# Optimization experiments

Hardware: AMD Instinct MI355X
Metric: run time of the kernel (lower is better)

The kernel has to match this reference:

```python
import jax, jax.numpy as jnp
import numpy as np

N, E, F_IN, H, L = 100000, 1600000, 256, 128, 4
ALPHA, THETA, EPS = 0.1, 0.5, 1e-5


def setup_inputs() -> dict:
    key = jax.random.key(0)
    ks = jax.random.split(key, 6)
    x = jax.random.normal(ks[0], (N, F_IN), dtype=jnp.float32)
    edge_index = jax.random.randint(ks[1], (2, E), 0, N, dtype=jnp.int32)
    lin0_w = jax.random.normal(ks[2], (F_IN, H), dtype=jnp.float32) / np.sqrt(F_IN)
    lin0_b = jnp.zeros((H,), dtype=jnp.float32)
    conv_w = jax.random.normal(ks[3], (L, H, H), dtype=jnp.float32) / np.sqrt(H)
    bn_gamma = jnp.ones((L - 1, H), dtype=jnp.float32)
    bn_beta = jnp.zeros((L - 1, H), dtype=jnp.float32)
    return {"x": x, "edge_index": edge_index, "lin0_w": lin0_w, "lin0_b": lin0_b,
            "conv_w": conv_w, "bn_gamma": bn_gamma, "bn_beta": bn_beta}


def reference(x, edge_index, lin0_w, lin0_b, conv_w, bn_gamma, bn_beta):
    n = x.shape[0]
    loops = jnp.arange(n, dtype=edge_index.dtype)
    row = jnp.concatenate([edge_index[0], loops])  # source
    col = jnp.concatenate([edge_index[1], loops])  # target
    # GCN symmetric normalization with self-loops: D^{-1/2}(A+I)D^{-1/2}
    deg = jax.ops.segment_sum(jnp.ones_like(col, dtype=x.dtype), col, num_segments=n)
    dinv = jnp.where(deg > 0, jax.lax.rsqrt(deg), 0.0)
    norm = (dinv[row] * dinv[col])[:, None]  # [E+N, 1]

    def prop(h):  # sparse aggregation: out[c] += norm * h[r]
        return jax.ops.segment_sum(h[row] * norm, col, num_segments=n)

    # GCNConv input layer
    z = prop(x @ lin0_w) + lin0_b
    x0 = z
    for i in range(L):
        h = prop(z)
        beta = float(np.log(THETA / (i + 1) + 1.0))
        s = (1.0 - ALPHA) * h + ALPHA * x0          # identity mapping to initial features
        z = (1.0 - beta) * s + beta * (s @ conv_w[i])  # shared_weights GCN2Conv
        if i < L - 1:
            mu = jnp.mean(z, axis=0)
            var = jnp.mean((z - mu) ** 2, axis=0)
            z = (z - mu) * jax.lax.rsqrt(var + EPS) * bn_gamma[i] + bn_beta[i]
            z = jax.nn.relu(z)
    return z
```

## Files before the change

kernel.cpp:

```cpp
#include <hip/hip_runtime.h>
#include <hip/hip_bf16.h>
#include <math.h>

#define H 128
#define EPS_BN 1e-5f
#define RSTATS 16

typedef __attribute__((ext_vector_type(8))) short short8;
typedef __attribute__((ext_vector_type(4))) float f32x4;

__device__ __forceinline__ float bf2f(ushort u){
  union { float f; uint v; } x; x.v = ((uint)u) << 16; return x.f;
}
__device__ __forceinline__ ushort f2bf(float f){
  union { float f; uint v; } x; x.f = f;
  uint v = x.v;
  uint r = v + 0x7fff + ((v >> 16) & 1);
  return (ushort)(r >> 16);
}

__device__ __forceinline__ void acc8(float* a, uint4 v, float wt){
  a[0] += wt*bf2f((ushort)(v.x & 0xffff)); a[1] += wt*bf2f((ushort)(v.x >> 16));
  a[2] += wt*bf2f((ushort)(v.y & 0xffff)); a[3] += wt*bf2f((ushort)(v.y >> 16));
  a[4] += wt*bf2f((ushort)(v.z & 0xffff)); a[5] += wt*bf2f((ushort)(v.z >> 16));
  a[6] += wt*bf2f((ushort)(v.w & 0xffff)); a[7] += wt*bf2f((ushort)(v.w >> 16));
}


__global__ void k_count(const int* __restrict__ col, int E, int* __restrict__ cnt){
  int i = blockIdx.x*blockDim.x + threadIdx.x;
  if (i < E) atomicAdd(&cnt[col[i]], 1);
}

__global__ void k_scan1(const int* __restrict__ cnt, int* __restrict__ off,
                        int* __restrict__ bsum, float* __restrict__ dinv, int n){
  __shared__ int s[1024];
  int t = threadIdx.x;
  int i = blockIdx.x*1024 + t;
  int v = (i < n) ? cnt[i] : 0;
  if (i < n) dinv[i] = rsqrtf((float)v + 1.0f);
  s[t] = v; __syncthreads();
  for (int d = 1; d < 1024; d <<= 1){
    int x = (t >= d) ? s[t-d] : 0;
    __syncthreads();
    s[t] += x;
    __syncthreads();
  }
  if (i < n) off[i] = s[t] - v;
  if (t == 1023) bsum[blockIdx.x] = s[1023];
}

__global__ void k_scan2(int* bsum, int nb){
  int l = threadIdx.x;
  int carry = 0;
  for (int b0 = 0; b0 < nb; b0 += 64){
    int i = b0 + l;
    int orig = (i < nb) ? bsum[i] : 0;
    int v = orig;
    #pragma unroll
    for (int d = 1; d < 64; d <<= 1){
      int x = __shfl_up(v, d);
      if (l >= d) v += x;
    }
    if (i < nb) bsum[i] = carry + v - orig;
    carry += __shfl(v, 63);
  }
}

__global__ void k_scan3(int* __restrict__ off, int* __restrict__ cursor,
                        const int* __restrict__ bsum, int n, int Etot){
  int i = blockIdx.x*blockDim.x + threadIdx.x;
  if (i < n){ int o = off[i] + bsum[i >> 10]; off[i] = o; cursor[i] = o; }
  if (i == 0) off[n] = Etot;
}

__global__ void k_fill(const int* __restrict__ row, const int* __restrict__ col, int E,
                       const float* __restrict__ dinv, int* __restrict__ cursor,
                       uint2* __restrict__ edge){
  int i = blockIdx.x*blockDim.x + threadIdx.x;
  if (i < E){
    int c = col[i], r = row[i];
    int p = atomicAdd(&cursor[c], 1);
    edge[p] = make_uint2((uint)r, __float_as_uint(dinv[r]*dinv[c]));
  }
}


__global__ __launch_bounds__(1024) void k_dhist(
    const int* __restrict__ cnt, int* __restrict__ dh, int n){
  __shared__ int lh[256];
  int t = threadIdx.x;
  if (t < 256) lh[t] = 0;
  __syncthreads();
  int i = blockIdx.x*1024 + t;
  if (i < n){
    int d = cnt[i]; if (d > 255) d = 255;
    atomicAdd(&lh[d], 1);
  }
  __syncthreads();
  if (t < 256 && lh[t]) atomicAdd(&dh[t], lh[t]);
}

__global__ void k_dscan(int* __restrict__ dh){
  __shared__ int s[256];
  int t = threadIdx.x;
  int v = dh[t];
  s[t] = v; __syncthreads();
  for (int d = 1; d < 256; d <<= 1){
    int x = (t >= d) ? s[t-d] : 0;
    __syncthreads();
    s[t] += x;
    __syncthreads();
  }
  dh[t] = s[t] - v;
}

__global__ __launch_bounds__(1024) void k_dperm(
    const int* __restrict__ cnt, int* __restrict__ dh,
    int* __restrict__ perm, int n){
  __shared__ int lh[256];
  __shared__ int lbase[256];
  int t = threadIdx.x;
  if (t < 256) lh[t] = 0;
  __syncthreads();
  int i = blockIdx.x*1024 + t;
  int d = 0, li = 0;
  if (i < n){
    d = cnt[i]; if (d > 255) d = 255;
    li = atomicAdd(&lh[d], 1);
  }
  __syncthreads();
  if (t < 256){
    int c = lh[t];
    lbase[t] = c ? atomicAdd(&dh[t], c) : 0;
  }
  __syncthreads();
  if (i < n) perm[lbase[d] + li] = i;
}


__global__ void k_prepw(const float* __restrict__ lin0_w, const float* __restrict__ conv_w,
                        ushort* __restrict__ lin0T, ushort* __restrict__ WpT,
                        float b0, float b1, float b2, float b3){
  int i = blockIdx.x*blockDim.x + threadIdx.x;
  if (i < 128*256){
    int nn = i >> 8, k = i & 255;
    lin0T[i] = f2bf(lin0_w[k*128 + nn]);
  } else if (i < 128*256 + 4*128*128){
    int j = i - 128*256;
    int ll = j >> 14, rc = j & 16383;
    int nn = rc >> 7, k = rc & 127;
    float beta = (ll==0)?b0:(ll==1)?b1:(ll==2)?b2:b3;
    float v = beta * conv_w[ll*16384 + k*128 + nn];
    if (k == nn) v += 1.0f - beta;
    WpT[j] = f2bf(v);
  }
}


__device__ __forceinline__ void gather_edges(
    float* a, const ushort* __restrict__ zin, const uint2* __restrict__ edge,
    int e0, int e1, int lr){
  int e = e0;
  for (; e + 3 < e1; e += 4){
    uint2 er0 = edge[e],   er1 = edge[e+1];
    uint2 er2 = edge[e+2], er3 = edge[e+3];
    uint4 v0 = *(const uint4*)(zin + (size_t)er0.x*H + lr*8);
    uint4 v1 = *(const uint4*)(zin + (size_t)er1.x*H + lr*8);
    uint4 v2 = *(const uint4*)(zin + (size_t)er2.x*H + lr*8);
    uint4 v3 = *(const uint4*)(zin + (size_t)er3.x*H + lr*8);
    acc8(a, v0, __uint_as_float(er0.y));
    acc8(a, v1, __uint_as_float(er1.y));
    acc8(a, v2, __uint_as_float(er2.y));
    acc8(a, v3, __uint_as_float(er3.y));
  }
  for (; e < e1; ++e){
    uint2 er = edge[e];
    uint4 v = *(const uint4*)(zin + (size_t)er.x*H + lr*8);
    acc8(a, v, __uint_as_float(er.y));
  }
}


__global__ __launch_bounds__(256) void k_prop0(
    const ushort* __restrict__ h, const int* __restrict__ off,
    const uint2* __restrict__ edge, const float* __restrict__ dinv,
    const float* __restrict__ bias,
    ushort* __restrict__ x0, int n){
  int gq = (blockIdx.x*blockDim.x + threadIdx.x) >> 4;
  if (gq >= n) return;
  int lr = threadIdx.x & 15;
  float a[8];
  #pragma unroll
  for (int j = 0; j < 8; ++j) a[j] = 0.f;
  float wc = dinv[gq]; wc *= wc;
  uint4 vs = *(const uint4*)(h + (size_t)gq*H + lr*8);
  gather_edges(a, h, edge, off[gq], off[gq+1], lr);
  acc8(a, vs, wc);
  float4 b0 = *(const float4*)(bias + lr*8);
  float4 b1 = *(const float4*)(bias + lr*8 + 4);
  uint4 pk;
  pk.x = (uint)f2bf(a[0]+b0.x) | ((uint)f2bf(a[1]+b0.y) << 16);
  pk.y = (uint)f2bf(a[2]+b0.z) | ((uint)f2bf(a[3]+b0.w) << 16);
  pk.z = (uint)f2bf(a[4]+b1.x) | ((uint)f2bf(a[5]+b1.y) << 16);
  pk.w = (uint)f2bf(a[6]+b1.z) | ((uint)f2bf(a[7]+b1.w) << 16);
  *(uint4*)(x0 + (size_t)gq*H + lr*8) = pk;
}


template<bool STATS, bool OUTF32, bool SAMEX0>
__global__ __launch_bounds__(256) void k_layer(
    const ushort* __restrict__ zin, const ushort* __restrict__ x0,
    const int* __restrict__ off, const uint2* __restrict__ edge,
    const float* __restrict__ dinv, const ushort* __restrict__ BT,
    const int* __restrict__ perm,
    void* __restrict__ zout, float* __restrict__ stats, int n)
{
  __shared__ ushort Sm[32*128];
  __shared__ int pm[32];
  int t = threadIdx.x;
  int w = t >> 6, l = t & 63;
  int lr = l & 15, q = l >> 4;
  int base = blockIdx.x * 32;
  if (t < 32) pm[t] = (base + t < n) ? perm[base + t] : -1;
  __syncthreads();

  #pragma unroll
  for (int g2 = 0; g2 < 2; ++g2){
    int row  = w*8 + g2*4 + q;
    int node = pm[row];
    float a[8];
    #pragma unroll
    for (int j = 0; j < 8; ++j) a[j] = 0.f;
    uint4 pk = make_uint4(0u,0u,0u,0u);
    if (node >= 0){
      float wc = dinv[node]; wc *= wc;
      uint4 vs = *(const uint4*)(zin + (size_t)node*H + lr*8);
      gather_edges(a, zin, edge, off[node], off[node+1], lr);
      acc8(a, vs, wc);
      uint4 xv = SAMEX0 ? vs : *(const uint4*)(x0 + (size_t)node*H + lr*8);
      float s0 = 0.9f*a[0] + 0.1f*bf2f((ushort)(xv.x & 0xffff));
      float s1 = 0.9f*a[1] + 0.1f*bf2f((ushort)(xv.x >> 16));
      float s2 = 0.9f*a[2] + 0.1f*bf2f((ushort)(xv.y & 0xffff));
      float s3 = 0.9f*a[3] + 0.1f*bf2f((ushort)(xv.y >> 16));
      float s4 = 0.9f*a[4] + 0.1f*bf2f((ushort)(xv.z & 0xffff));
      float s5 = 0.9f*a[5] + 0.1f*bf2f((ushort)(xv.z >> 16));
      float s6 = 0.9f*a[6] + 0.1f*bf2f((ushort)(xv.w & 0xffff));
      float s7 = 0.9f*a[7] + 0.1f*bf2f((ushort)(xv.w >> 16));
      pk.x = (uint)f2bf(s0) | ((uint)f2bf(s1) << 16);
      pk.y = (uint)f2bf(s2) | ((uint)f2bf(s3) << 16);
      pk.z = (uint)f2bf(s4) | ((uint)f2bf(s5) << 16);
      pk.w = (uint)f2bf(s6) | ((uint)f2bf(s7) << 16);
    }
    *(uint4*)(&Sm[row*128 + ((lr ^ (row & 15))*8)]) = pk;
  }

  short8 bfr[2][4];
  #pragma unroll
  for (int c = 0; c < 2; ++c)
    #pragma unroll
    for (int ks = 0; ks < 4; ++ks)
      bfr[c][ks] = *(const short8*)(BT + (size_t)(w*32 + c*16 + lr)*H + ks*32 + q*8);

  __syncthreads();

  f32x4 acc[2][2];
  #pragma unroll
  for (int rt = 0; rt < 2; ++rt){
    acc[rt][0] = (f32x4){0.f,0.f,0.f,0.f};
    acc[rt][1] = (f32x4){0.f,0.f,0.f,0.f};
  }
  #pragma unroll
  for (int rt = 0; rt < 2; ++rt){
    int row = rt*16 + lr;
    #pragma unroll
    for (int ks = 0; ks < 4; ++ks){
      short8 af = *(const short8*)(&Sm[row*128 + (((ks*4 + q) ^ (row & 15))*8)]);
      acc[rt][0] = __builtin_amdgcn_mfma_f32_16x16x32_bf16(af, bfr[0][ks], acc[rt][0], 0,0,0);
      acc[rt][1] = __builtin_amdgcn_mfma_f32_16x16x32_bf16(af, bfr[1][ks], acc[rt][1], 0,0,0);
    }
  }

  #pragma unroll
  for (int rt = 0; rt < 2; ++rt){
    #pragma unroll
    for (int c = 0; c < 2; ++c){
      #pragma unroll
      for (int j2 = 0; j2 < 4; ++j2){
        int rowl = rt*16 + q*4 + j2;
        int nodeo = pm[rowl];
        float v = acc[rt][c][j2];
        if (OUTF32){
          if (nodeo >= 0)
            ((float*)zout)[(size_t)nodeo*H + w*32 + c*16 + lr] = v;
        } else {
          float other = __shfl(v, l ^ 1);
          if (!(lr & 1) && nodeo >= 0){
            uint pk = (uint)f2bf(v) | ((uint)f2bf(other) << 16);
            ((uint*)zout)[(size_t)nodeo*64 + w*16 + c*8 + (lr >> 1)] = pk;
          }
        }
      }
    }
  }
  if (STATS){
    #pragma unroll
    for (int c = 0; c < 2; ++c){
      float sv = 0.f, sq = 0.f;
      #pragma unroll
      for (int rt = 0; rt < 2; ++rt)
        #pragma unroll
        for (int j2 = 0; j2 < 4; ++j2){
          float v = acc[rt][c][j2];
          sv += v; sq += v*v;
        }
      sv += __shfl(sv, l ^ 16); sv += __shfl(sv, l ^ 32);
      sq += __shfl(sq, l ^ 16); sq += __shfl(sq, l ^ 32);
      if (q == 0){
        float* st = stats + (size_t)(blockIdx.x & (RSTATS-1))*256;
        atomicAdd(&st[w*32 + c*16 + lr], sv);
        atomicAdd(&st[128 + w*32 + c*16 + lr], sq);
      }
    }
  }
}


__global__ void k_bnfinal(float* __restrict__ stats, const float* __restrict__ gamma,
                          const float* __restrict__ beta, float* __restrict__ scsh,
                          float inv_n){
  int f = threadIdx.x;
  float s = 0.f, s2 = 0.f;
  for (int r = 0; r < RSTATS; ++r){
    s  += stats[r*256 + f];
    s2 += stats[r*256 + 128 + f];
    stats[r*256 + f] = 0.f;
    stats[r*256 + 128 + f] = 0.f;
  }
  float mu  = s * inv_n;
  float var = s2 * inv_n - mu*mu;
  float sc  = rsqrtf(var + EPS_BN) * gamma[f];
  scsh[f]       = sc;
  scsh[128 + f] = beta[f] - mu*sc;
}


__global__ __launch_bounds__(256) void k_bnapply(
    uint4* __restrict__ z, const float* __restrict__ scsh, int n16){
  int i = blockIdx.x*blockDim.x + threadIdx.x;
  if (i >= n16) return;
  int f8 = (i & 15) * 8;
  uint4 v = z[i];
  uint r[4];
  #pragma unroll
  for (int p = 0; p < 4; ++p){
    uint  u  = (&v.x)[p];
    float z0 = bf2f((ushort)(u & 0xffff));
    float z1 = bf2f((ushort)(u >> 16));
    float y0 = fmaxf(fmaf(z0, scsh[f8 + p*2],     scsh[128 + f8 + p*2]),     0.f);
    float y1 = fmaxf(fmaf(z1, scsh[f8 + p*2 + 1], scsh[128 + f8 + p*2 + 1]), 0.f);
    r[p] = (uint)f2bf(y0) | ((uint)f2bf(y1) << 16);
  }
  z[i] = make_uint4(r[0], r[1], r[2], r[3]);
}


__global__ __launch_bounds__(256) void k_gemm0(
    const float* __restrict__ Af, const ushort* __restrict__ BT,
    ushort* __restrict__ Cb, int n){
  const int K = 256;
  __shared__ ushort As[64*32];
  __shared__ ushort Bs[128*32];
  int t = threadIdx.x;
  int br = blockIdx.x * 64;
  int w = t >> 6, l = t & 63;
  int lr = l & 15, lk = l >> 4;
  int swz = (lr >> 1) & 3;

  f32x4 acc[8];
  #pragma unroll
  for (int i = 0; i < 8; ++i) acc[i] = (f32x4){0.f,0.f,0.f,0.f};

  int sar = t >> 2;
  int sab = t & 3;
  int sa_off = sar*32 + ((sab ^ ((sar>>1)&3))*8);

  for (int k0 = 0; k0 < K; k0 += 32){
    int grow = br + sar;
    float4 v0 = make_float4(0.f,0.f,0.f,0.f), v1 = v0;
    if (grow < n){
      v0 = *(const float4*)(Af + (size_t)grow*K + k0 + sab*8);
      v1 = *(const float4*)(Af + (size_t)grow*K + k0 + sab*8 + 4);
    }
    ushort tmp[8] = {f2bf(v0.x),f2bf(v0.y),f2bf(v0.z),f2bf(v0.w),
                     f2bf(v1.x),f2bf(v1.y),f2bf(v1.z),f2bf(v1.w)};
    *(uint4*)(&As[sa_off]) = *(const uint4*)tmp;
    #pragma unroll
    for (int i = 0; i < 2; ++i){
      int qq = t + i*256;
      int nrow = qq >> 2, bb = qq & 3;
      uint4 v = *(const uint4*)(BT + (size_t)nrow*K + k0 + bb*8);
      *(uint4*)(&Bs[nrow*32 + ((bb ^ ((nrow>>1)&3))*8)]) = v;
    }
    __syncthreads();
    short8 af = *(const short8*)(&As[(w*16+lr)*32 + ((lk ^ swz)*8)]);
    #pragma unroll
    for (int tn = 0; tn < 8; ++tn){
      short8 bfv = *(const short8*)(&Bs[(tn*16+lr)*32 + ((lk ^ swz)*8)]);
      acc[tn] = __builtin_amdgcn_mfma_f32_16x16x32_bf16(af, bfv, acc[tn], 0, 0, 0);
    }
    __syncthreads();
  }
  int orow = br + w*16 + lk*4;
  #pragma unroll
  for (int tn = 0; tn < 8; ++tn){
    #pragma unroll
    for (int j = 0; j < 4; ++j){
      float mine  = acc[tn][j];
      float other = __shfl(mine, l ^ 1);
      if (!(l & 1) && (orow + j) < n){
        uint pk = (uint)f2bf(mine) | ((uint)f2bf(other) << 16);
        ((uint*)Cb)[(size_t)(orow+j)*64 + tn*8 + (lr >> 1)] = pk;
      }
    }
  }
}


extern "C" void kernel_launch(void* const* d_in, const int* in_sizes, int n_in,
                              void* d_out, int out_size, void* d_ws, size_t ws_size,
                              hipStream_t stream){
  const float* x        = (const float*)d_in[0];
  const int*   ei       = (const int*)  d_in[1];
  const float* lin0_w   = (const float*)d_in[2];
  const float* lin0_b   = (const float*)d_in[3];
  const float* conv_w   = (const float*)d_in[4];
  const float* bn_gamma = (const float*)d_in[5];
  const float* bn_beta  = (const float*)d_in[6];
  float* out = (float*)d_out;

  int N = in_sizes[0] / 256;
  int E = in_sizes[1] / 2;
  const int* row = ei;
  const int* col = ei + E;

  char* ws = (char*)d_ws;
  size_t p = 0;
  auto alloc = [&](size_t bytes)->char*{
    char* r = ws + p; p = (p + bytes + 255) & ~(size_t)255; return r;
  };
  int*    cnt    = (int*)   alloc((size_t)N*4);
  int*    off    = (int*)   alloc((size_t)(N+1)*4);
  int*    cursor = (int*)   alloc((size_t)N*4);
  float*  dinv   = (float*) alloc((size_t)N*4);
  int*    bsum   = (int*)   alloc(512*4);
  int*    dh     = (int*)   alloc(256*4);
  int*    perm   = (int*)   alloc((size_t)N*4);
  uint2*  edge   = (uint2*) alloc((size_t)E*8);
  ushort* zb     = (ushort*)alloc((size_t)N*H*2);
  ushort* sb     = (ushort*)alloc((size_t)N*H*2);
  ushort* x0b    = (ushort*)alloc((size_t)N*H*2);
  ushort* lin0T  = (ushort*)alloc(128*256*2);
  ushort* WpT    = (ushort*)alloc(4*128*128*2);
  float*  stats  = (float*) alloc(RSTATS*256*4);
  float*  scsh   = (float*) alloc(2*128*4);

  float betas[4];
  for (int i = 0; i < 4; ++i) betas[i] = logf(0.5f/(float)(i+1) + 1.0f);
  float inv_n = 1.0f/(float)N;

  hipMemsetAsync(cnt, 0, (size_t)N*4, stream);
  hipMemsetAsync(dh, 0, 256*4, stream);
  k_count<<<(E+255)/256, 256, 0, stream>>>(col, E, cnt);
  int nb1k = (N + 1023)/1024;
  k_dhist<<<nb1k, 1024, 0, stream>>>(cnt, dh, N);
  k_dscan<<<1, 256, 0, stream>>>(dh);
  k_dperm<<<nb1k, 1024, 0, stream>>>(cnt, dh, perm, N);
  k_scan1<<<nb1k, 1024, 0, stream>>>(cnt, off, bsum, dinv, N);
  k_scan2<<<1, 64, 0, stream>>>(bsum, nb1k);
  k_scan3<<<(N+255)/256, 256, 0, stream>>>(off, cursor, bsum, N, E);
  k_fill <<<(E+255)/256, 256, 0, stream>>>(row, col, E, dinv, cursor, edge);

  k_prepw<<<(128*256 + 4*128*128 + 255)/256, 256, 0, stream>>>(
      lin0_w, conv_w, lin0T, WpT, betas[0], betas[1], betas[2], betas[3]);

  int gemm_blocks = (N + 63)/64;
  int lay_blocks  = (N + 31)/32;
  int prop_blocks = (N + 15)/16;
  int bn_blocks   = ((N*16) + 255)/256;

  k_gemm0<<<gemm_blocks, 256, 0, stream>>>(x, lin0T, sb, N);
  k_prop0<<<prop_blocks, 256, 0, stream>>>(sb, off, edge, dinv, lin0_b, x0b, N);

  hipMemsetAsync(stats, 0, RSTATS*256*4, stream);

  k_layer<true,false,true><<<lay_blocks, 256, 0, stream>>>(
      x0b, x0b, off, edge, dinv, WpT + 0*128*128, perm, sb, stats, N);
  k_bnfinal<<<1, 128, 0, stream>>>(stats, bn_gamma + 0*H, bn_beta + 0*H, scsh, inv_n);
  k_bnapply<<<bn_blocks, 256, 0, stream>>>((uint4*)sb, scsh, N*16);

  k_layer<true,false,false><<<lay_blocks, 256, 0, stream>>>(
      sb, x0b, off, edge, dinv, WpT + 1*128*128, perm, zb, stats, N);
  k_bnfinal<<<1, 128, 0, stream>>>(stats, bn_gamma + 1*H, bn_beta + 1*H, scsh, inv_n);
  k_bnapply<<<bn_blocks, 256, 0, stream>>>((uint4*)zb, scsh, N*16);

  k_layer<true,false,false><<<lay_blocks, 256, 0, stream>>>(
      zb, x0b, off, edge, dinv, WpT + 2*128*128, perm, sb, stats, N);
  k_bnfinal<<<1, 128, 0, stream>>>(stats, bn_gamma + 2*H, bn_beta + 2*H, scsh, inv_n);
  k_bnapply<<<bn_blocks, 256, 0, stream>>>((uint4*)sb, scsh, N*16);

  k_layer<false,true,false><<<lay_blocks, 256, 0, stream>>>(
      sb, x0b, off, edge, dinv, WpT + 3*128*128, perm, out, nullptr, N);
}
```

Measured before the change: 596.1 us.

## Pre-bucket edges by target range before CSR fill; degree-permute prop0

CSR construction now runs a two-pass bucketing step. Edges are first scattered into 64 coarse buckets by target id (col>>11) in a temp buffer that aliases zb. The fill kernel then reads them in bucket order, with XCD-aware block remapping, so the cursor atomics and edge writes hit localized memory regions instead of random ones. prop0 also walks nodes in degree-sorted perm order to balance work across wavefronts. This adds two extra passes over the edge list and extra launches in exchange for better atomic and write locality.

```diff
diff --git a/kernel.cpp b/kernel.cpp
--- a/kernel.cpp
+++ b/kernel.cpp
@@ -74,14 +74,71 @@
   if (i == 0) off[n] = Etot;
 }
 
-__global__ void k_fill(const int* __restrict__ row, const int* __restrict__ col, int E,
-                       const float* __restrict__ dinv, int* __restrict__ cursor,
-                       uint2* __restrict__ edge){
-  int i = blockIdx.x*blockDim.x + threadIdx.x;
+
+__global__ __launch_bounds__(1024) void k_bcount(
+    const int* __restrict__ col, int E, int* __restrict__ bh){
+  __shared__ int lh[64];
+  int t = threadIdx.x;
+  if (t < 64) lh[t] = 0;
+  __syncthreads();
+  int i = blockIdx.x*1024 + t;
   if (i < E){
-    int c = col[i], r = row[i];
+    int b = col[i] >> 11; if (b > 63) b = 63;
+    atomicAdd(&lh[b], 1);
+  }
+  __syncthreads();
+  if (t < 64 && lh[t]) atomicAdd(&bh[t], lh[t]);
+}
+
+__global__ void k_bscan(int* __restrict__ bh){
+  int l = threadIdx.x;
+  int v = bh[l];
+  int s = v;
+  #pragma unroll
+  for (int d = 1; d < 64; d <<= 1){
+    int x = __shfl_up(s, d);
+    if (l >= d) s += x;
+  }
+  bh[l] = s - v;
+}
+
+__global__ __launch_bounds__(1024) void k_bucket(
+    const int* __restrict__ row, const int* __restrict__ col, int E,
+    int* __restrict__ bcur, uint2* __restrict__ tmp){
+  __shared__ int lh[64];
+  __shared__ int lbase[64];
+  int t = threadIdx.x;
+  if (t < 64) lh[t] = 0;
+  __syncthreads();
+  int i = blockIdx.x*1024 + t;
+  int b = 0, li = 0, r = 0, c = 0;
+  if (i < E){
+    r = row[i]; c = col[i];
+    b = c >> 11; if (b > 63) b = 63;
+    li = atomicAdd(&lh[b], 1);
+  }
+  __syncthreads();
+  if (t < 64){
+    int cc = lh[t];
+    lbase[t] = cc ? atomicAdd(&bcur[t], cc) : 0;
+  }
+  __syncthreads();
+  if (i < E) tmp[lbase[b] + li] = make_uint2((uint)r, (uint)c);
+}
+
+__global__ __launch_bounds__(256) void k_fill2(
+    const uint2* __restrict__ tmp, int E, const float* __restrict__ dinv,
+    int* __restrict__ cursor, uint2* __restrict__ edge, int nwg){
+  int bid = blockIdx.x;
+  int qq = nwg >> 3, rr = nwg & 7;
+  int xcd = bid & 7, idx = bid >> 3;
+  int wg = (xcd < rr ? xcd*(qq+1) : rr*(qq+1) + (xcd-rr)*qq) + idx;
+  int i = wg*256 + threadIdx.x;
+  if (i < E){
+    uint2 rc = tmp[i];
+    int r = (int)rc.x, c = (int)rc.y;
     int p = atomicAdd(&cursor[c], 1);
-    edge[p] = make_uint2((uint)r, __float_as_uint(dinv[r]*dinv[c]));
+    edge[p] = make_uint2(rc.x, __float_as_uint(dinv[r]*dinv[c]));
   }
 }
 
@@ -185,10 +242,11 @@
 __global__ __launch_bounds__(256) void k_prop0(
     const ushort* __restrict__ h, const int* __restrict__ off,
     const uint2* __restrict__ edge, const float* __restrict__ dinv,
-    const float* __restrict__ bias,
+    const float* __restrict__ bias, const int* __restrict__ perm,
     ushort* __restrict__ x0, int n){
-  int gq = (blockIdx.x*blockDim.x + threadIdx.x) >> 4;
-  if (gq >= n) return;
+  int pq = (blockIdx.x*blockDim.x + threadIdx.x) >> 4;
+  if (pq >= n) return;
+  int gq = perm[pq];
   int lr = threadIdx.x & 15;
   float a[8];
   #pragma unroll
@@ -455,6 +513,7 @@
   float*  dinv   = (float*) alloc((size_t)N*4);
   int*    bsum   = (int*)   alloc(512*4);
   int*    dh     = (int*)   alloc(256*4);
+  int*    bh     = (int*)   alloc(64*4);
   int*    perm   = (int*)   alloc((size_t)N*4);
   uint2*  edge   = (uint2*) alloc((size_t)E*8);
   ushort* zb     = (ushort*)alloc((size_t)N*H*2);
@@ -465,21 +524,29 @@
   float*  stats  = (float*) alloc(RSTATS*256*4);
   float*  scsh   = (float*) alloc(2*128*4);
 
+  uint2* tmp = (uint2*)zb;
+
   float betas[4];
   for (int i = 0; i < 4; ++i) betas[i] = logf(0.5f/(float)(i+1) + 1.0f);
   float inv_n = 1.0f/(float)N;
 
   hipMemsetAsync(cnt, 0, (size_t)N*4, stream);
   hipMemsetAsync(dh, 0, 256*4, stream);
+  hipMemsetAsync(bh, 0, 64*4, stream);
   k_count<<<(E+255)/256, 256, 0, stream>>>(col, E, cnt);
+  int eb1k = (E + 1023)/1024;
   int nb1k = (N + 1023)/1024;
+  k_bcount<<<eb1k, 1024, 0, stream>>>(col, E, bh);
+  k_bscan<<<1, 64, 0, stream>>>(bh);
   k_dhist<<<nb1k, 1024, 0, stream>>>(cnt, dh, N);
   k_dscan<<<1, 256, 0, stream>>>(dh);
   k_dperm<<<nb1k, 1024, 0, stream>>>(cnt, dh, perm, N);
   k_scan1<<<nb1k, 1024, 0, stream>>>(cnt, off, bsum, dinv, N);
   k_scan2<<<1, 64, 0, stream>>>(bsum, nb1k);
   k_scan3<<<(N+255)/256, 256, 0, stream>>>(off, cursor, bsum, N, E);
-  k_fill <<<(E+255)/256, 256, 0, stream>>>(row, col, E, dinv, cursor, edge);
+  k_bucket<<<eb1k, 1024, 0, stream>>>(row, col, E, bh, tmp);
+  int f2wg = (E + 255)/256;
+  k_fill2<<<f2wg, 256, 0, stream>>>(tmp, E, dinv, cursor, edge, f2wg);
 
   k_prepw<<<(128*256 + 4*128*128 + 255)/256, 256, 0, stream>>>(
       lin0_w, conv_w, lin0T, WpT, betas[0], betas[1], betas[2], betas[3]);
@@ -490,7 +557,7 @@
   int bn_blocks   = ((N*16) + 255)/256;
 
   k_gemm0<<<gemm_blocks, 256, 0, stream>>>(x, lin0T, sb, N);
-  k_prop0<<<prop_blocks, 256, 0, stream>>>(sb, off, edge, dinv, lin0_b, x0b, N);
+  k_prop0<<<prop_blocks, 256, 0, stream>>>(sb, off, edge, dinv, lin0_b, perm, x0b, N);
 
   hipMemsetAsync(stats, 0, RSTATS*256*4, stream);
 
```

Result: slower. 681.5 us (+14.3%).
